# Kernel optimization log

Measured on AMD Instinct MI355X. Metric: run time of the kernel, lower is better.

Reference implementation:

```python
import jax, jax.numpy as jnp
import numpy as np

ALPHA = 100.0  # soft-assignment sharpness (init kwarg)
EPS = 1e-12    # F.normalize eps


def _l2norm(v, axis):
    n = jnp.sqrt(jnp.sum(v * v, axis=axis, keepdims=True))
    return v / jnp.maximum(n, EPS)


def setup_inputs() -> dict:
    key = jax.random.key(0)
    k1, k2 = jax.random.split(key)
    x = jax.random.normal(k1, (32, 128, 128, 128), dtype=jnp.float32)
    centroids = jax.random.uniform(k2, (64, 128), dtype=jnp.float32)
    return {"x": x, "centroids": centroids}


def reference(x, centroids):
    # x: [N, C, H, W], centroids: [K, C]
    N, C, H, W = x.shape
    K = centroids.shape[0]
    # descriptor-wise L2 normalization over channel dim
    xn = _l2norm(x, axis=1)
    xf = xn.reshape(N, C, H * W)  # [N, C, S]
    # 1x1 conv == per-pixel linear: weight = 2*alpha*centroids, bias = -alpha*||c_k||
    w = 2.0 * ALPHA * centroids                     # [K, C]
    b = -ALPHA * jnp.linalg.norm(centroids, axis=1)  # [K]
    logits = jnp.einsum('kc,ncs->nks', w, xf) + b[None, :, None]
    a = jax.nn.softmax(logits, axis=1)  # soft assignment over clusters, [N, K, S]
    # VLAD: sum_s a[n,k,s] * (x[n,:,s] - c[k,:]) expressed as one matmul + rank-1 term
    vlad = jnp.einsum('nks,ncs->nkc', a, xf) - a.sum(-1)[:, :, None] * centroids[None]
    vlad = _l2norm(vlad, axis=2)          # intra-normalization
    vlad = vlad.reshape(N, K * C)
    vlad = _l2norm(vlad, axis=1)          # global L2 normalization
    return vlad
```

## Files before the change

kernel.cpp:

```cpp
#include <hip/hip_runtime.h>
#include <hip/hip_bf16.h>


#define NIMG 32
#define C 128
#define S 16384
#define K 64
#define SPLITS 32
#define SPAN 512
#define PXC 64
#define XTP 136
#define AP 72
#define XP 40

typedef short bf16x8 __attribute__((ext_vector_type(8)));
typedef float f32x4 __attribute__((ext_vector_type(4)));

__device__ __forceinline__ unsigned short f2bf(float f) {
    union { __hip_bfloat16 h; unsigned short u; } v;
    v.h = __float2bfloat16(f);
    return v.u;
}
__device__ __forceinline__ float bf2f(unsigned short u) {
    return __uint_as_float(((unsigned int)u) << 16);
}

__global__ __launch_bounds__(256) void k_prep(const float* __restrict__ cent,
                                              float* __restrict__ bvec) {
    int t = threadIdx.x;
    if (t < K) {
        float ss = 0.f;
        for (int c = 0; c < C; ++c) { float v = cent[t * C + c]; ss += v * v; }
        bvec[t] = -100.0f * sqrtf(ss);
    }
}

#define SMEM_BYTES 47104

__global__ __launch_bounds__(256, 3) void k_main(const float* __restrict__ x,
                                                 const float* __restrict__ cent,
                                                 const float* __restrict__ bvec,
                                                 float* __restrict__ part,
                                                 float* __restrict__ asum_p) {
    __shared__ __align__(16) char smem[SMEM_BYTES];
    unsigned short* xTh   = (unsigned short*)(smem);
    unsigned short* xTl   = (unsigned short*)(smem + 17408);
    unsigned short* x_lds = (unsigned short*)(smem + 17408);
    unsigned short* a_lds = (unsigned short*)(smem + 34816);
    float* ssq_part       = (float*)(smem + 44032);
    float* redA           = (float*)(smem + 45056);
    float* redB           = (float*)(smem + 46080);

    int n = blockIdx.x >> 5;
    int sp = blockIdx.x & 31;
    int t = threadIdx.x, l = t & 63, w = t >> 6;
    int kw = 16 * w, l15 = l & 15, lhi = l >> 4;

    const float* xn_img = x + (size_t)n * C * S;

    bf16x8 wh[4], wl[4];
#pragma unroll
    for (int cs = 0; cs < 4; ++cs) {
        const float* wrow = cent + (kw + l15) * C + cs * 32 + 8 * lhi;
#pragma unroll
        for (int e = 0; e < 8; ++e) {
            float wv = 200.0f * wrow[e];
            unsigned short h = f2bf(wv);
            wh[cs][e] = (short)h;
            wl[cs][e] = (short)f2bf(wv - bf2f(h));
        }
    }
    float bias[4];
#pragma unroll
    for (int j = 0; j < 4; ++j) bias[j] = bvec[kw + 4 * lhi + j];

    f32x4 acc[8];
#pragma unroll
    for (int i = 0; i < 8; ++i) acc[i] = (f32x4){0.f, 0.f, 0.f, 0.f};
    float asumacc[4] = {0.f, 0.f, 0.f, 0.f};

    for (int ch = 0; ch < SPAN / PXC; ++ch) {
        int pxbase = sp * SPAN + ch * PXC;
        __syncthreads();

        {
            int px = t & 63, cq = t >> 6;
            const float* xcol = xn_img + (size_t)(cq * 32) * S + pxbase + px;
            float sa = 0.f, sb = 0.f;
#pragma unroll
            for (int u = 0; u < 4; ++u) {
                unsigned int bh[4], bl[4];
#pragma unroll
                for (int e = 0; e < 4; ++e) {
                    float v0 = xcol[(size_t)(u * 8 + 2 * e) * S];
                    float v1 = xcol[(size_t)(u * 8 + 2 * e + 1) * S];
                    sa = fmaf(v0, v0, sa);
                    sb = fmaf(v1, v1, sb);
                    unsigned short h0 = f2bf(v0), h1 = f2bf(v1);
                    unsigned short l0 = f2bf(v0 - bf2f(h0));
                    unsigned short l1 = f2bf(v1 - bf2f(h1));
                    bh[e] = (unsigned int)h0 | ((unsigned int)h1 << 16);
                    bl[e] = (unsigned int)l0 | ((unsigned int)l1 << 16);
                }
                int c0 = cq * 32 + u * 8;
                uint4 vh = {bh[0], bh[1], bh[2], bh[3]};
                uint4 vl = {bl[0], bl[1], bl[2], bl[3]};
                *(uint4*)(&xTh[px * XTP + c0]) = vh;
                *(uint4*)(&xTl[px * XTP + c0]) = vl;
            }
            ssq_part[cq * 64 + px] = sa + sb;
        }
        __syncthreads();

        f32x4 lgacc[4];
#pragma unroll
        for (int t4 = 0; t4 < 4; ++t4) lgacc[t4] = (f32x4){0.f, 0.f, 0.f, 0.f};
#pragma unroll
        for (int t4 = 0; t4 < 4; ++t4) {
#pragma unroll
            for (int cs = 0; cs < 4; ++cs) {
                int boff = (16 * t4 + l15) * XTP + cs * 32 + 8 * lhi;
                bf16x8 bh = *(const bf16x8*)(&xTh[boff]);
                bf16x8 bl = *(const bf16x8*)(&xTl[boff]);
                lgacc[t4] = __builtin_amdgcn_mfma_f32_16x16x32_bf16(wh[cs], bh, lgacc[t4], 0, 0, 0);
                lgacc[t4] = __builtin_amdgcn_mfma_f32_16x16x32_bf16(wh[cs], bl, lgacc[t4], 0, 0, 0);
                lgacc[t4] = __builtin_amdgcn_mfma_f32_16x16x32_bf16(wl[cs], bh, lgacc[t4], 0, 0, 0);
            }
        }

        float invt[4];
#pragma unroll
        for (int t4 = 0; t4 < 4; ++t4) {
            int px = 16 * t4 + l15;
            float s = ssq_part[px] + ssq_part[64 + px] + ssq_part[128 + px] + ssq_part[192 + px];
            invt[t4] = 1.0f / fmaxf(sqrtf(s), 1e-12f);
        }
        float lg[4][4];
        float pmax[4];
#pragma unroll
        for (int t4 = 0; t4 < 4; ++t4) {
            float m = -3.4e38f;
#pragma unroll
            for (int j = 0; j < 4; ++j) {
                lg[t4][j] = fmaf(lgacc[t4][j], invt[t4], bias[j]);
                m = fmaxf(m, lg[t4][j]);
            }
            pmax[t4] = m;
        }
#pragma unroll
        for (int t4 = 0; t4 < 4; ++t4) {
            pmax[t4] = fmaxf(pmax[t4], __shfl_xor(pmax[t4], 16));
            pmax[t4] = fmaxf(pmax[t4], __shfl_xor(pmax[t4], 32));
        }
        if (l < 16) {
#pragma unroll
            for (int t4 = 0; t4 < 4; ++t4) redA[(16 * t4 + l15) * 4 + w] = pmax[t4];
        }
        __syncthreads();
        float psum[4];
#pragma unroll
        for (int t4 = 0; t4 < 4; ++t4) {
            float4 mv = *(const float4*)(&redA[(16 * t4 + l15) * 4]);
            float m = fmaxf(fmaxf(mv.x, mv.y), fmaxf(mv.z, mv.w));
            float s = 0.f;
#pragma unroll
            for (int j = 0; j < 4; ++j) {
                float p = __expf(lg[t4][j] - m);
                lg[t4][j] = p;
                s += p;
            }
            psum[t4] = s;
        }
#pragma unroll
        for (int t4 = 0; t4 < 4; ++t4) {
            psum[t4] += __shfl_xor(psum[t4], 16);
            psum[t4] += __shfl_xor(psum[t4], 32);
        }
        if (l < 16) {
#pragma unroll
            for (int t4 = 0; t4 < 4; ++t4) redB[(16 * t4 + l15) * 4 + w] = psum[t4];
        }
        __syncthreads();
#pragma unroll
        for (int t4 = 0; t4 < 4; ++t4) {
            float4 sv = *(const float4*)(&redB[(16 * t4 + l15) * 4]);
            float rs = 1.0f / (sv.x + sv.y + sv.z + sv.w);
            float inv = invt[t4];
#pragma unroll
            for (int j = 0; j < 4; ++j) {
                float a = lg[t4][j] * rs;
                asumacc[j] += a;
                a_lds[(kw + 4 * lhi + j) * AP + 16 * t4 + l15] = f2bf(a * inv);
            }
        }

        for (int sc = 0; sc < 2; ++sc) {
            __syncthreads();
            {
                int c = t >> 1, half = t & 1;
                const float4* xsrc = (const float4*)(xn_img + (size_t)c * S + pxbase + 32 * sc + 16 * half);
                unsigned int uu[8];
#pragma unroll
                for (int q = 0; q < 4; ++q) {
                    float4 xv = xsrc[q];
                    unsigned short b0 = f2bf(xv.x), b1 = f2bf(xv.y);
                    unsigned short b2 = f2bf(xv.z), b3 = f2bf(xv.w);
                    uu[2 * q]     = (unsigned int)b0 | ((unsigned int)b1 << 16);
                    uu[2 * q + 1] = (unsigned int)b2 | ((unsigned int)b3 << 16);
                }
                uint4 w0 = {uu[0], uu[1], uu[2], uu[3]};
                uint4 w1 = {uu[4], uu[5], uu[6], uu[7]};
                *(uint4*)(&x_lds[c * XP + 16 * half])     = w0;
                *(uint4*)(&x_lds[c * XP + 16 * half + 8]) = w1;
            }
            __syncthreads();
            bf16x8 af = *(const bf16x8*)(&a_lds[(kw + l15) * AP + 32 * sc + 8 * lhi]);
#pragma unroll
            for (int nt = 0; nt < 8; ++nt) {
                bf16x8 bfv = *(const bf16x8*)(&x_lds[(16 * nt + l15) * XP + 8 * lhi]);
                acc[nt] = __builtin_amdgcn_mfma_f32_16x16x32_bf16(af, bfv, acc[nt], 0, 0, 0);
            }
        }
    }

    size_t pbase = (size_t)(n * SPLITS + sp) * K * C;
#pragma unroll
    for (int nt = 0; nt < 8; ++nt) {
#pragma unroll
        for (int j = 0; j < 4; ++j) {
            int row = kw + 4 * lhi + j;
            int col = 16 * nt + l15;
            part[pbase + (size_t)row * C + col] = acc[nt][j];
        }
    }
#pragma unroll
    for (int j = 0; j < 4; ++j) {
        float v = asumacc[j];
        v += __shfl_xor(v, 1);
        v += __shfl_xor(v, 2);
        v += __shfl_xor(v, 4);
        v += __shfl_xor(v, 8);
        if (l15 == 0)
            asum_p[(size_t)(n * SPLITS + sp) * K + kw + 4 * lhi + j] = v;
    }
}

__global__ __launch_bounds__(256) void k_reduce(const float* __restrict__ part,
                                                const float* __restrict__ asum_p,
                                                const float* __restrict__ cent,
                                                float* __restrict__ vlad_red,
                                                float* __restrict__ ssq) {
    __shared__ float asum_l[K];
    int n = blockIdx.x >> 3;
    int cg = blockIdx.x & 7;
    int t = threadIdx.x;

    if (t < K) {
        float s = 0.f;
        for (int sp = 0; sp < SPLITS; ++sp) s += asum_p[(size_t)(n * SPLITS + sp) * K + t];
        asum_l[t] = s;
    }
    __syncthreads();

    int cell4 = cg * 256 + t;
    int k = (cell4 * 4) >> 7;
    float4 acc = {0.f, 0.f, 0.f, 0.f};
    for (int sp = 0; sp < SPLITS; ++sp) {
        const float4* p = (const float4*)(part + (size_t)(n * SPLITS + sp) * K * C);
        float4 v = p[cell4];
        acc.x += v.x; acc.y += v.y; acc.z += v.z; acc.w += v.w;
    }
    float am = asum_l[k];
    const float4 cv = ((const float4*)cent)[cell4];
    acc.x -= am * cv.x; acc.y -= am * cv.y;
    acc.z -= am * cv.z; acc.w -= am * cv.w;
    ((float4*)vlad_red)[(size_t)n * 2048 + cell4] = acc;

    float sq = acc.x * acc.x + acc.y * acc.y + acc.z * acc.z + acc.w * acc.w;
#pragma unroll
    for (int st = 16; st >= 1; st >>= 1) sq += __shfl_xor(sq, st);
    if ((t & 31) == 0) ssq[n * K + k] = sq;
}

__global__ __launch_bounds__(256) void k_final(const float* __restrict__ vlad_red,
                                               const float* __restrict__ ssq,
                                               float* __restrict__ out) {
    __shared__ float ri_l[K];
    __shared__ float ssn[K];
    __shared__ float gi_s;
    int n = blockIdx.x, t = threadIdx.x;

    if (t < K) {
        float ss = ssq[n * K + t];
        float ri = 1.0f / fmaxf(sqrtf(ss), 1e-12f);
        ri_l[t] = ri;
        ssn[t] = ss * ri * ri;
    }
    __syncthreads();
    if (t == 0) {
        float g = 0.f;
        for (int k = 0; k < K; ++k) g += ssn[k];
        gi_s = 1.0f / fmaxf(sqrtf(g), 1e-12f);
    }
    __syncthreads();
    float gi = gi_s;
    for (int c4 = t; c4 < 2048; c4 += 256) {
        float4 v = ((const float4*)vlad_red)[(size_t)n * 2048 + c4];
        float r = ri_l[c4 >> 5] * gi;
        v.x *= r; v.y *= r; v.z *= r; v.w *= r;
        ((float4*)out)[(size_t)n * 2048 + c4] = v;
    }
}

extern "C" void kernel_launch(void* const* d_in, const int* in_sizes, int n_in,
                              void* d_out, int out_size, void* d_ws, size_t ws_size,
                              hipStream_t stream) {
    const float* x = (const float*)d_in[0];
    const float* cent = (const float*)d_in[1];
    float* out = (float*)d_out;
    char* ws = (char*)d_ws;

    float* bvec     = (float*)(ws);
    float* part     = (float*)(ws + (1u << 20));
    float* asum_p   = (float*)(ws + (34u << 20));
    float* vlad_red = (float*)(ws + (35u << 20));
    float* ssq      = (float*)(ws + (36u << 20));

    hipLaunchKernelGGL(k_prep,   dim3(1),             dim3(256), 0, stream, cent, bvec);
    hipLaunchKernelGGL(k_main,   dim3(NIMG * SPLITS), dim3(256), 0, stream, x, cent, bvec, part, asum_p);
    hipLaunchKernelGGL(k_reduce, dim3(NIMG * 8),      dim3(256), 0, stream, part, asum_p, cent, vlad_red, ssq);
    hipLaunchKernelGGL(k_final,  dim3(NIMG),          dim3(256), 0, stream, vlad_red, ssq, out);
}
```

Before: 425.8 us.

## Swizzle LDS layouts, prefetch x tile early, and stage full chunk once

Replaces the padded LDS strides with an XOR swizzle so all buffers are unpadded. The global loads of the x chunk for the VLAD matmul are issued before the logits phase and held in registers, so their latency overlaps the MFMA and softmax work. The two half-chunk staging passes are merged into one 64-pixel write, which removes two barriers per chunk. The cost is 32 extra VGPRs of prefetched data live across the softmax, which may pressure occupancy at 3 blocks per CU.

```diff
diff --git a/kernel.cpp b/kernel.cpp
--- a/kernel.cpp
+++ b/kernel.cpp
@@ -9,9 +9,8 @@
 #define SPLITS 32
 #define SPAN 512
 #define PXC 64
-#define XTP 136
-#define AP 72
-#define XP 40
+
+#define SWZ7(row, e) ((e) ^ (((row) & 7) << 3))
 
 typedef short bf16x8 __attribute__((ext_vector_type(8)));
 typedef float f32x4 __attribute__((ext_vector_type(4)));
@@ -35,7 +34,7 @@
     }
 }
 
-#define SMEM_BYTES 47104
+#define SMEM_BYTES 44032
 
 __global__ __launch_bounds__(256, 3) void k_main(const float* __restrict__ x,
                                                  const float* __restrict__ cent,
@@ -44,17 +43,18 @@
                                                  float* __restrict__ asum_p) {
     __shared__ __align__(16) char smem[SMEM_BYTES];
     unsigned short* xTh   = (unsigned short*)(smem);
-    unsigned short* xTl   = (unsigned short*)(smem + 17408);
-    unsigned short* x_lds = (unsigned short*)(smem + 17408);
-    unsigned short* a_lds = (unsigned short*)(smem + 34816);
-    float* ssq_part       = (float*)(smem + 44032);
-    float* redA           = (float*)(smem + 45056);
-    float* redB           = (float*)(smem + 46080);
+    unsigned short* xTl   = (unsigned short*)(smem + 16384);
+    unsigned short* x_lds = (unsigned short*)(smem + 16384);
+    unsigned short* a_lds = (unsigned short*)(smem + 32768);
+    float* ssq_part       = (float*)(smem + 40960);
+    float* redA           = (float*)(smem + 41984);
+    float* redB           = (float*)(smem + 43008);
 
     int n = blockIdx.x >> 5;
     int sp = blockIdx.x & 31;
     int t = threadIdx.x, l = t & 63, w = t >> 6;
     int kw = 16 * w, l15 = l & 15, lhi = l >> 4;
+    int swl = (l15 & 7) << 3;
 
     const float* xn_img = x + (size_t)n * C * S;
 
@@ -79,12 +79,14 @@
     for (int i = 0; i < 8; ++i) acc[i] = (f32x4){0.f, 0.f, 0.f, 0.f};
     float asumacc[4] = {0.f, 0.f, 0.f, 0.f};
 
+    int px = t & 63, cq = t >> 6;
+    int cF = t >> 1, halfF = t & 1;
+
     for (int ch = 0; ch < SPAN / PXC; ++ch) {
         int pxbase = sp * SPAN + ch * PXC;
         __syncthreads();
 
         {
-            int px = t & 63, cq = t >> 6;
             const float* xcol = xn_img + (size_t)(cq * 32) * S + pxbase + px;
             float sa = 0.f, sb = 0.f;
 #pragma unroll
@@ -102,14 +104,21 @@
                     bh[e] = (unsigned int)h0 | ((unsigned int)h1 << 16);
                     bl[e] = (unsigned int)l0 | ((unsigned int)l1 << 16);
                 }
-                int c0 = cq * 32 + u * 8;
+                int eo = px * 128 + SWZ7(px, cq * 32 + u * 8);
                 uint4 vh = {bh[0], bh[1], bh[2], bh[3]};
                 uint4 vl = {bl[0], bl[1], bl[2], bl[3]};
-                *(uint4*)(&xTh[px * XTP + c0]) = vh;
-                *(uint4*)(&xTl[px * XTP + c0]) = vl;
+                *(uint4*)(&xTh[eo]) = vh;
+                *(uint4*)(&xTl[eo]) = vl;
             }
             ssq_part[cq * 64 + px] = sa + sb;
         }
+
+        float4 xq[8];
+        {
+            const float4* xf4 = (const float4*)(xn_img + (size_t)cF * S + pxbase + 32 * halfF);
+#pragma unroll
+            for (int u = 0; u < 8; ++u) xq[u] = xf4[u];
+        }
         __syncthreads();
 
         f32x4 lgacc[4];
@@ -119,7 +128,7 @@
         for (int t4 = 0; t4 < 4; ++t4) {
 #pragma unroll
             for (int cs = 0; cs < 4; ++cs) {
-                int boff = (16 * t4 + l15) * XTP + cs * 32 + 8 * lhi;
+                int boff = (16 * t4 + l15) * 128 + ((cs * 32 + 8 * lhi) ^ swl);
                 bf16x8 bh = *(const bf16x8*)(&xTh[boff]);
                 bf16x8 bl = *(const bf16x8*)(&xTl[boff]);
                 lgacc[t4] = __builtin_amdgcn_mfma_f32_16x16x32_bf16(wh[cs], bh, lgacc[t4], 0, 0, 0);
@@ -131,8 +140,8 @@
         float invt[4];
 #pragma unroll
         for (int t4 = 0; t4 < 4; ++t4) {
-            int px = 16 * t4 + l15;
-            float s = ssq_part[px] + ssq_part[64 + px] + ssq_part[128 + px] + ssq_part[192 + px];
+            int p = 16 * t4 + l15;
+            float s = ssq_part[p] + ssq_part[64 + p] + ssq_part[128 + p] + ssq_part[192 + p];
             invt[t4] = 1.0f / fmaxf(sqrtf(s), 1e-12f);
         }
         float lg[4][4];
@@ -157,6 +166,23 @@
             for (int t4 = 0; t4 < 4; ++t4) redA[(16 * t4 + l15) * 4 + w] = pmax[t4];
         }
         __syncthreads();
+
+        {
+#pragma unroll
+            for (int u = 0; u < 4; ++u) {
+                float4 a0 = xq[2 * u], a1 = xq[2 * u + 1];
+                unsigned short b0 = f2bf(a0.x), b1 = f2bf(a0.y);
+                unsigned short b2 = f2bf(a0.z), b3 = f2bf(a0.w);
+                unsigned short b4 = f2bf(a1.x), b5 = f2bf(a1.y);
+                unsigned short b6 = f2bf(a1.z), b7 = f2bf(a1.w);
+                uint4 pv = {(unsigned int)b0 | ((unsigned int)b1 << 16),
+                            (unsigned int)b2 | ((unsigned int)b3 << 16),
+                            (unsigned int)b4 | ((unsigned int)b5 << 16),
+                            (unsigned int)b6 | ((unsigned int)b7 << 16)};
+                *(uint4*)(&x_lds[cF * 64 + SWZ7(cF, 32 * halfF + 8 * u)]) = pv;
+            }
+        }
+
         float psum[4];
 #pragma unroll
         for (int t4 = 0; t4 < 4; ++t4) {
@@ -181,43 +207,30 @@
             for (int t4 = 0; t4 < 4; ++t4) redB[(16 * t4 + l15) * 4 + w] = psum[t4];
         }
         __syncthreads();
+
 #pragma unroll
         for (int t4 = 0; t4 < 4; ++t4) {
             float4 sv = *(const float4*)(&redB[(16 * t4 + l15) * 4]);
             float rs = 1.0f / (sv.x + sv.y + sv.z + sv.w);
             float inv = invt[t4];
+            int p = 16 * t4 + l15;
 #pragma unroll
             for (int j = 0; j < 4; ++j) {
                 float a = lg[t4][j] * rs;
                 asumacc[j] += a;
-                a_lds[(kw + 4 * lhi + j) * AP + 16 * t4 + l15] = f2bf(a * inv);
-            }
-        }
-
+                int k = kw + 4 * lhi + j;
+                a_lds[k * 64 + SWZ7(k, p)] = f2bf(a * inv);
+            }
+        }
+        __syncthreads();
+
+#pragma unroll
         for (int sc = 0; sc < 2; ++sc) {
-            __syncthreads();
-            {
-                int c = t >> 1, half = t & 1;
-                const float4* xsrc = (const float4*)(xn_img + (size_t)c * S + pxbase + 32 * sc + 16 * half);
-                unsigned int uu[8];
-#pragma unroll
-                for (int q = 0; q < 4; ++q) {
-                    float4 xv = xsrc[q];
-                    unsigned short b0 = f2bf(xv.x), b1 = f2bf(xv.y);
-                    unsigned short b2 = f2bf(xv.z), b3 = f2bf(xv.w);
-                    uu[2 * q]     = (unsigned int)b0 | ((unsigned int)b1 << 16);
-                    uu[2 * q + 1] = (unsigned int)b2 | ((unsigned int)b3 << 16);
-                }
-                uint4 w0 = {uu[0], uu[1], uu[2], uu[3]};
-                uint4 w1 = {uu[4], uu[5], uu[6], uu[7]};
-                *(uint4*)(&x_lds[c * XP + 16 * half])     = w0;
-                *(uint4*)(&x_lds[c * XP + 16 * half + 8]) = w1;
-            }
-            __syncthreads();
-            bf16x8 af = *(const bf16x8*)(&a_lds[(kw + l15) * AP + 32 * sc + 8 * lhi]);
+            int eoff = (32 * sc + 8 * lhi) ^ swl;
+            bf16x8 af = *(const bf16x8*)(&a_lds[(kw + l15) * 64 + eoff]);
 #pragma unroll
             for (int nt = 0; nt < 8; ++nt) {
-                bf16x8 bfv = *(const bf16x8*)(&x_lds[(16 * nt + l15) * XP + 8 * lhi]);
+                bf16x8 bfv = *(const bf16x8*)(&x_lds[(16 * nt + l15) * 64 + eoff]);
                 acc[nt] = __builtin_amdgcn_mfma_f32_16x16x32_bf16(af, bfv, acc[nt], 0, 0, 0);
             }
         }
```

Result: slower. 543.1 us (+27.5%).
